# Optimization experiments

Hardware: AMD Instinct MI355X
Metric: run time of the kernel (lower is better)

The kernel has to match this reference:

```python
import jax, jax.numpy as jnp
import numpy as np

M, N, B, T = 512, 2048, 8192, 5
P, P_MAX = 0.012, 0.12


def setup_inputs() -> dict:
    key = jax.random.key(0)
    k1, k2 = jax.random.split(key)
    A = jax.random.normal(k1, (M, N), dtype=jnp.float32) / np.float32(np.sqrt(M))
    y = jax.random.normal(k2, (B, M), dtype=jnp.float32)
    # norm = 1.001 * ||A^T A||_2 (largest singular value), as in __init__
    norm = np.float32(1.001 * np.linalg.norm(np.asarray(A).T @ np.asarray(A), 2))
    beta = jnp.ones((T + 1, 1, 1), jnp.float32) * (np.float32(0.1) / norm)
    mu = jnp.ones((T + 1, 1, 1), jnp.float32) / norm
    W = A.T  # Linear weight overwritten with A.T; W(y) = y @ W.T = y @ A
    return {"y": y, "A": A, "W": W, "beta": beta, "mu": mu}


def _shrink(x, beta, t):
    # top-p hard-threshold with softshrink fallback
    abs_x = jnp.abs(x)
    idx = int(min(P * t, P_MAX) * x.shape[-1])  # static per unrolled step
    if idx > 0:
        thr = jax.lax.top_k(abs_x, idx)[0][:, idx - 1:idx]  # [B,1] p-th largest |x|
    else:
        thr = jnp.zeros((x.shape[0], 1), x.dtype)
    u = x / beta
    x_soft = beta * (jnp.sign(u) * jnp.maximum(jnp.abs(u) - 1.0, 0.0))  # beta*softshrink(x/beta,1)
    return jnp.where(abs_x >= thr, x, x_soft)


def reference(y, A, W, beta, mu):
    # W(v) = v @ W.T ; W initialized to A.T so W(y) = y @ A
    h = mu[0] * (y @ W.T)            # [B, N]
    x = _shrink(h, beta[0], 0)
    for t in range(1, T + 1):
        r = x @ A.T - y              # [B, M] residual
        k = mu[t] * (r @ W.T)        # [B, N]
        x = _shrink(x - k, beta[t], t)
    return x
```

## Files before the change

kernel.cpp:

```cpp
#include <hip/hip_runtime.h>


typedef int int4v __attribute__((ext_vector_type(4)));

__device__ __forceinline__ void quant2(float v, float inv_s,
                                       signed char& q1, signed char& q0) {
    int q = __float2int_rn(v * inv_s);
    q = q > 16256 ? 16256 : (q < -16256 ? -16256 : q);
    int hi = (q + 64) >> 7;
    q1 = (signed char)hi;
    q0 = (signed char)(q - (hi << 7));
}

__device__ __forceinline__ void gl_lds16(const signed char* g, signed char* lds) {
    __builtin_amdgcn_global_load_lds(
        (const __attribute__((address_space(1))) void*)g,
        (__attribute__((address_space(3))) void*)lds, 16, 0, 0);
}

template<int NJ, int EPI>
__global__ __launch_bounds__(256, 2) void gemm_i8(
    const signed char* __restrict__ A1, const signed char* __restrict__ A0, int lda,
    const signed char* __restrict__ B1, const signed char* __restrict__ B0, int ldb,
    const float* __restrict__ sAv,
    const float* __restrict__ sBv,
    const float* __restrict__ Yaux,
    float* __restrict__ outF,
    const float* __restrict__ muPtr, int muIdx, int K, int ldOut)
{
    constexpr int BN = 32 * NJ;
    __shared__ signed char As1[2][128 * 64];
    __shared__ signed char As0[2][128 * 64];
    __shared__ signed char Bs1[2][BN * 64];
    __shared__ signed char Bs0[2][BN * 64];

    const int tid  = threadIdx.x;
    const int wid  = tid >> 6;
    const int lane = tid & 63;
    const int quad = lane >> 4;
    const int l16  = lane & 15;
    const int waveM = (wid >> 1) * 64;
    const int waveN = (wid & 1) * (16 * NJ);
    const int swz   = (l16 >> 1) & 3;

    const int flat  = blockIdx.x + gridDim.x * blockIdx.y;
    const int mBase = (flat & 63) * 128;
    const int nBase = (flat >> 6) * BN;

    int4v accH[4][NJ] = {};
    int4v accM[4][NJ] = {};

    auto stage = [&](int b, int k0) {
        #pragma unroll
        for (int rr = 0; rr < 2; ++rr) {
            int c   = rr * 256 + tid;
            int row = c >> 2;
            int js  = (c & 3) ^ ((row >> 1) & 3);
            size_t ga = (size_t)(mBase + row) * lda + k0 + js * 16;
            size_t doff = (size_t)((rr * 256 + wid * 64) * 16);
            gl_lds16(A1 + ga, As1[b] + doff);
            gl_lds16(A0 + ga, As0[b] + doff);
        }
        #pragma unroll
        for (int rr = 0; rr < BN / 64; ++rr) {
            int c   = rr * 256 + tid;
            int row = c >> 2;
            int js  = (c & 3) ^ ((row >> 1) & 3);
            size_t gb = (size_t)(nBase + row) * ldb + k0 + js * 16;
            size_t doff = (size_t)((rr * 256 + wid * 64) * 16);
            gl_lds16(B1 + gb, Bs1[b] + doff);
            gl_lds16(B0 + gb, Bs0[b] + doff);
        }
    };

    const int KT = K >> 6;
    stage(0, 0);

    for (int kt = 0; kt < KT; ++kt) {
        const int cur = kt & 1;
        if (kt + 1 < KT) {
            stage(cur ^ 1, (kt + 1) << 6);
            if constexpr (NJ == 4) asm volatile("s_waitcnt vmcnt(8)" ::: "memory");
            else                   asm volatile("s_waitcnt vmcnt(6)" ::: "memory");
        } else {
            asm volatile("s_waitcnt vmcnt(0)" ::: "memory");
        }
        __builtin_amdgcn_s_barrier();

        int4v a1[4], a0[4], b1[NJ], b0[NJ];
        #pragma unroll
        for (int i = 0; i < 4; ++i) {
            int off = (waveM + i * 16 + l16) * 64 + ((quad ^ swz) * 16);
            a1[i] = *(const int4v*)(&As1[cur][off]);
            a0[i] = *(const int4v*)(&As0[cur][off]);
        }
        #pragma unroll
        for (int j = 0; j < NJ; ++j) {
            int off = (waveN + j * 16 + l16) * 64 + ((quad ^ swz) * 16);
            b1[j] = *(const int4v*)(&Bs1[cur][off]);
            b0[j] = *(const int4v*)(&Bs0[cur][off]);
        }
        __builtin_amdgcn_s_setprio(1);
        #pragma unroll
        for (int i = 0; i < 4; ++i)
            #pragma unroll
            for (int j = 0; j < NJ; ++j) {
                accH[i][j] = __builtin_amdgcn_mfma_i32_16x16x64_i8(a1[i], b1[j], accH[i][j], 0, 0, 0);
                accM[i][j] = __builtin_amdgcn_mfma_i32_16x16x64_i8(a1[i], b0[j], accM[i][j], 0, 0, 0);
                accM[i][j] = __builtin_amdgcn_mfma_i32_16x16x64_i8(a0[i], b1[j], accM[i][j], 0, 0, 0);
            }
        __builtin_amdgcn_s_setprio(0);
        __builtin_amdgcn_s_barrier();
    }

    const float mu = muPtr[muIdx];
    #pragma unroll
    for (int i = 0; i < 4; ++i) {
        #pragma unroll
        for (int j = 0; j < NJ; ++j) {
            const int gr0 = mBase + waveM + i * 16 + quad * 4;
            const int gc  = nBase + waveN + j * 16 + l16;
            const float sB = sBv[gc];
            #pragma unroll
            for (int r2 = 0; r2 < 4; ++r2) {
                const int    gr  = gr0 + r2;
                const size_t idx = (size_t)gr * ldOut + gc;
                const float  sA  = sAv[gr];
                float v = sA * sB * ((float)accH[i][j][r2] * 16384.f
                                   + (float)accM[i][j][r2] * 128.f);
                if constexpr (EPI == 0)      outF[idx] = mu * v;
                else if constexpr (EPI == 1) outF[idx] = v - Yaux[idx];
                else                         outF[idx] = Yaux[idx] - mu * v;
            }
        }
    }
}

template<int COLS>
__global__ __launch_bounds__(256) void rowquant_kernel(
    const float* __restrict__ src,
    signed char* __restrict__ q1, signed char* __restrict__ q0,
    float* __restrict__ scale)
{
    const int wid  = threadIdx.x >> 6;
    const int lane = threadIdx.x & 63;
    const long long row = (long long)blockIdx.x * 4 + wid;
    constexpr int EP = COLS / 256;
    const float* s = src + row * COLS;

    float v[EP * 4];
    #pragma unroll
    for (int c = 0; c < EP; ++c) {
        float4 f = ((const float4*)s)[c * 64 + lane];
        v[c * 4 + 0] = f.x; v[c * 4 + 1] = f.y; v[c * 4 + 2] = f.z; v[c * 4 + 3] = f.w;
    }
    float mx = 0.f;
    #pragma unroll
    for (int i = 0; i < EP * 4; ++i) mx = fmaxf(mx, fabsf(v[i]));
    #pragma unroll
    for (int off = 32; off >= 1; off >>= 1) mx = fmaxf(mx, __shfl_xor(mx, off, 64));
    mx = fmaxf(mx, 1e-20f);
    if (lane == 0) scale[row] = mx / 16256.f;
    const float inv = 16256.f / mx;

    #pragma unroll
    for (int c = 0; c < EP; ++c) {
        size_t col = (size_t)(c * 64 + lane) * 4;
        signed char h[4], l[4];
        #pragma unroll
        for (int e = 0; e < 4; ++e) quant2(v[c * 4 + e], inv, h[e], l[e]);
        *(char4*)(q1 + row * COLS + col) = *(char4*)h;
        *(char4*)(q0 + row * COLS + col) = *(char4*)l;
    }
}

__global__ __launch_bounds__(256) void shrink_kernel(
    float* __restrict__ z,
    signed char* __restrict__ X1, signed char* __restrict__ X0,
    float* __restrict__ sX,
    const float* __restrict__ betaPtr, int tIdx, int kSel, int writeF32)
{
    const int wid  = threadIdx.x >> 6;
    const int lane = threadIdx.x & 63;
    const long long row = (long long)blockIdx.x * 4 + wid;
    float* zr = z + row * 2048;

    float v[32];
    #pragma unroll
    for (int c = 0; c < 8; ++c) {
        float4 f = ((const float4*)zr)[c * 64 + lane];
        v[c * 4 + 0] = f.x; v[c * 4 + 1] = f.y; v[c * 4 + 2] = f.z; v[c * 4 + 3] = f.w;
    }

    if (kSel > 0) {
        const float beta = betaPtr[tIdx];
        unsigned a[32];
        #pragma unroll
        for (int i = 0; i < 32; ++i) a[i] = __float_as_uint(fabsf(v[i]));

        unsigned lo = 0u, hi = 0x7F800000u;
        for (int it = 0; it < 31; ++it) {
            unsigned mid = (lo + hi) >> 1;
            int cnt = 0;
            #pragma unroll
            for (int i = 0; i < 32; ++i) cnt += (a[i] >= mid) ? 1 : 0;
            #pragma unroll
            for (int off = 32; off >= 1; off >>= 1) cnt += __shfl_xor(cnt, off, 64);
            if (cnt >= kSel) lo = mid; else hi = mid;
        }
        const unsigned thr = lo;
        #pragma unroll
        for (int i = 0; i < 32; ++i) {
            if (a[i] < thr) {
                float av   = __uint_as_float(a[i]);
                float soft = fmaxf(av - beta, 0.f);
                v[i] = copysignf(soft, v[i]);
            }
        }
    }

    float mx = 0.f;
    #pragma unroll
    for (int i = 0; i < 32; ++i) mx = fmaxf(mx, fabsf(v[i]));
    #pragma unroll
    for (int off = 32; off >= 1; off >>= 1) mx = fmaxf(mx, __shfl_xor(mx, off, 64));
    mx = fmaxf(mx, 1e-20f);
    if (lane == 0) sX[row] = mx / 16256.f;
    const float inv = 16256.f / mx;

    #pragma unroll
    for (int c = 0; c < 8; ++c) {
        size_t col = (size_t)(c * 64 + lane) * 4;
        signed char h[4], l[4];
        #pragma unroll
        for (int e = 0; e < 4; ++e) quant2(v[c * 4 + e], inv, h[e], l[e]);
        *(char4*)(X1 + row * 2048 + col) = *(char4*)h;
        *(char4*)(X0 + row * 2048 + col) = *(char4*)l;
        if (writeF32) {
            float4 f;
            f.x = v[c * 4 + 0]; f.y = v[c * 4 + 1]; f.z = v[c * 4 + 2]; f.w = v[c * 4 + 3];
            ((float4*)zr)[c * 64 + lane] = f;
        }
    }
}

extern "C" void kernel_launch(void* const* d_in, const int* in_sizes, int n_in,
                              void* d_out, int out_size, void* d_ws, size_t ws_size,
                              hipStream_t stream)
{
    const float* y    = (const float*)d_in[0];
    const float* A    = (const float*)d_in[1];
    const float* W    = (const float*)d_in[2];
    const float* beta = (const float*)d_in[3];
    const float* mu   = (const float*)d_in[4];
    float* out = (float*)d_out;

    signed char* A1q  = (signed char*)d_ws;
    signed char* A0q  = A1q  + 512 * 2048;
    signed char* AT1q = A0q  + 512 * 2048;
    signed char* AT0q = AT1q + 2048 * 512;
    signed char* y1q  = AT0q + 2048 * 512;
    signed char* y0q  = y1q  + 8192 * 512;
    signed char* x1q  = y0q  + 8192 * 512;
    signed char* x0q  = x1q  + (size_t)8192 * 2048;
    signed char* r1q  = x0q  + (size_t)8192 * 2048;
    signed char* r0q  = r1q  + 8192 * 512;
    float* rF  = (float*)(r0q + 8192 * 512);
    float* sa  = rF + (size_t)8192 * 512;
    float* sat = sa  + 512;
    float* sy  = sat + 2048;
    float* sx  = sy  + 8192;
    float* sr  = sx  + 8192;

    rowquant_kernel<2048><<<128, 256, 0, stream>>>(A, A1q, A0q, sa);
    rowquant_kernel<512><<<512, 256, 0, stream>>>(W, AT1q, AT0q, sat);
    rowquant_kernel<512><<<2048, 256, 0, stream>>>(y, y1q, y0q, sy);

    gemm_i8<4, 0><<<dim3(16, 64), 256, 0, stream>>>(
        y1q, y0q, 512, AT1q, AT0q, 512, sy, sat,
        nullptr, out, mu, 0, 512, 2048);
    shrink_kernel<<<2048, 256, 0, stream>>>(out, x1q, x0q, sx, beta, 0, 0, 0);

    for (int t = 1; t <= 5; ++t) {
        double p = 0.012 * t; if (p > 0.12) p = 0.12;
        int kSel = (int)(p * 2048.0);

        gemm_i8<2, 1><<<dim3(8, 64), 256, 0, stream>>>(
            x1q, x0q, 2048, A1q, A0q, 2048, sx, sa,
            y, rF, mu, t, 2048, 512);
        rowquant_kernel<512><<<2048, 256, 0, stream>>>(rF, r1q, r0q, sr);

        gemm_i8<4, 2><<<dim3(16, 64), 256, 0, stream>>>(
            r1q, r0q, 512, AT1q, AT0q, 512, sr, sat,
            out, out, mu, t, 512, 2048);

        shrink_kernel<<<2048, 256, 0, stream>>>(out, x1q, x0q, sx, beta, t, kSel, 1);
    }
}
```

Baseline: 798.1 us.

## Process two rows per wave in shrink and skip final quantized plane writes

```diff
diff --git a/kernel.cpp b/kernel.cpp
--- a/kernel.cpp
+++ b/kernel.cpp
@@ -178,68 +178,124 @@
     float* __restrict__ z,
     signed char* __restrict__ X1, signed char* __restrict__ X0,
     float* __restrict__ sX,
-    const float* __restrict__ betaPtr, int tIdx, int kSel, int writeF32)
+    const float* __restrict__ betaPtr, int tIdx, int kSel,
+    int writeF32, int writePlanes)
 {
     const int wid  = threadIdx.x >> 6;
     const int lane = threadIdx.x & 63;
-    const long long row = (long long)blockIdx.x * 4 + wid;
-    float* zr = z + row * 2048;
-
-    float v[32];
+    const long long r0 = (long long)blockIdx.x * 8 + wid * 2;
+    float* z0 = z + r0 * 2048;
+    float* z1 = z0 + 2048;
+
+    unsigned a0[32], a1[32];
+    unsigned s0 = 0, s1 = 0;
     #pragma unroll
     for (int c = 0; c < 8; ++c) {
-        float4 f = ((const float4*)zr)[c * 64 + lane];
-        v[c * 4 + 0] = f.x; v[c * 4 + 1] = f.y; v[c * 4 + 2] = f.z; v[c * 4 + 3] = f.w;
+        float4 f0 = ((const float4*)z0)[c * 64 + lane];
+        float4 f1 = ((const float4*)z1)[c * 64 + lane];
+        const float e0[4] = {f0.x, f0.y, f0.z, f0.w};
+        const float e1[4] = {f1.x, f1.y, f1.z, f1.w};
+        #pragma unroll
+        for (int e = 0; e < 4; ++e) {
+            unsigned b0 = __float_as_uint(e0[e]);
+            unsigned b1 = __float_as_uint(e1[e]);
+            s0 |= (b0 >> 31) << (c * 4 + e);
+            s1 |= (b1 >> 31) << (c * 4 + e);
+            a0[c * 4 + e] = b0 & 0x7FFFFFFFu;
+            a1[c * 4 + e] = b1 & 0x7FFFFFFFu;
+        }
     }
 
     if (kSel > 0) {
         const float beta = betaPtr[tIdx];
-        unsigned a[32];
-        #pragma unroll
-        for (int i = 0; i < 32; ++i) a[i] = __float_as_uint(fabsf(v[i]));
-
-        unsigned lo = 0u, hi = 0x7F800000u;
+        unsigned lo0 = 0u, hi0 = 0x7F800000u;
+        unsigned lo1 = 0u, hi1 = 0x7F800000u;
         for (int it = 0; it < 31; ++it) {
-            unsigned mid = (lo + hi) >> 1;
-            int cnt = 0;
+            const unsigned m0 = (lo0 + hi0) >> 1;
+            const unsigned m1 = (lo1 + hi1) >> 1;
+            int c0 = 0, c1 = 0;
             #pragma unroll
-            for (int i = 0; i < 32; ++i) cnt += (a[i] >= mid) ? 1 : 0;
+            for (int i = 0; i < 32; ++i) {
+                c0 += (a0[i] >= m0) ? 1 : 0;
+                c1 += (a1[i] >= m1) ? 1 : 0;
+            }
+            int pk = c0 | (c1 << 16);
             #pragma unroll
-            for (int off = 32; off >= 1; off >>= 1) cnt += __shfl_xor(cnt, off, 64);
-            if (cnt >= kSel) lo = mid; else hi = mid;
-        }
-        const unsigned thr = lo;
+            for (int off = 32; off >= 1; off >>= 1) pk += __shfl_xor(pk, off, 64);
+            if ((pk & 0xFFFF) >= kSel) lo0 = m0; else hi0 = m0;
+            if ((pk >> 16)    >= kSel) lo1 = m1; else hi1 = m1;
+        }
+        const unsigned thr0 = lo0, thr1 = lo1;
         #pragma unroll
         for (int i = 0; i < 32; ++i) {
-            if (a[i] < thr) {
-                float av   = __uint_as_float(a[i]);
-                float soft = fmaxf(av - beta, 0.f);
-                v[i] = copysignf(soft, v[i]);
-            }
-        }
-    }
-
-    float mx = 0.f;
-    #pragma unroll
-    for (int i = 0; i < 32; ++i) mx = fmaxf(mx, fabsf(v[i]));
-    #pragma unroll
-    for (int off = 32; off >= 1; off >>= 1) mx = fmaxf(mx, __shfl_xor(mx, off, 64));
-    mx = fmaxf(mx, 1e-20f);
-    if (lane == 0) sX[row] = mx / 16256.f;
-    const float inv = 16256.f / mx;
+            float af0 = __uint_as_float(a0[i]);
+            float af1 = __uint_as_float(a1[i]);
+            unsigned sf0 = __float_as_uint(fmaxf(af0 - beta, 0.f));
+            unsigned sf1 = __float_as_uint(fmaxf(af1 - beta, 0.f));
+            a0[i] = (a0[i] >= thr0) ? a0[i] : sf0;
+            a1[i] = (a1[i] >= thr1) ? a1[i] : sf1;
+        }
+    }
+
+    unsigned mx0 = 0u, mx1 = 0u;
+    #pragma unroll
+    for (int i = 0; i < 32; ++i) {
+        mx0 = a0[i] > mx0 ? a0[i] : mx0;
+        mx1 = a1[i] > mx1 ? a1[i] : mx1;
+    }
+    #pragma unroll
+    for (int off = 32; off >= 1; off >>= 1) {
+        unsigned t0 = (unsigned)__shfl_xor((int)mx0, off, 64);
+        unsigned t1 = (unsigned)__shfl_xor((int)mx1, off, 64);
+        mx0 = t0 > mx0 ? t0 : mx0;
+        mx1 = t1 > mx1 ? t1 : mx1;
+    }
+    const float fm0 = fmaxf(__uint_as_float(mx0), 1e-20f);
+    const float fm1 = fmaxf(__uint_as_float(mx1), 1e-20f);
+    if (writePlanes && lane == 0) {
+        sX[r0]     = fm0 / 16256.f;
+        sX[r0 + 1] = fm1 / 16256.f;
+    }
+    const float inv0 = 16256.f / fm0;
+    const float inv1 = 16256.f / fm1;
 
     #pragma unroll
     for (int c = 0; c < 8; ++c) {
-        size_t col = (size_t)(c * 64 + lane) * 4;
-        signed char h[4], l[4];
-        #pragma unroll
-        for (int e = 0; e < 4; ++e) quant2(v[c * 4 + e], inv, h[e], l[e]);
-        *(char4*)(X1 + row * 2048 + col) = *(char4*)h;
-        *(char4*)(X0 + row * 2048 + col) = *(char4*)l;
+        const size_t col = (size_t)(c * 64 + lane) * 4;
+        signed char h0[4], l0[4], h1[4], l1[4];
+        float w0[4], w1[4];
+        #pragma unroll
+        for (int e = 0; e < 4; ++e) {
+            const int i = c * 4 + e;
+            const unsigned sg0 = (s0 >> i) & 1u;
+            const unsigned sg1 = (s1 >> i) & 1u;
+            const float av0 = __uint_as_float(a0[i]);
+            const float av1 = __uint_as_float(a1[i]);
+            w0[e] = __uint_as_float(a0[i] | (sg0 << 31));
+            w1[e] = __uint_as_float(a1[i] | (sg1 << 31));
+            int q0i = __float2int_rn(av0 * inv0);
+            int q1i = __float2int_rn(av1 * inv1);
+            q0i = q0i > 16256 ? 16256 : q0i;
+            q1i = q1i > 16256 ? 16256 : q1i;
+            q0i = sg0 ? -q0i : q0i;
+            q1i = sg1 ? -q1i : q1i;
+            int hi0b = (q0i + 64) >> 7;
+            int hi1b = (q1i + 64) >> 7;
+            h0[e] = (signed char)hi0b;  l0[e] = (signed char)(q0i - (hi0b << 7));
+            h1[e] = (signed char)hi1b;  l1[e] = (signed char)(q1i - (hi1b << 7));
+        }
+        if (writePlanes) {
+            *(char4*)(X1 + r0 * 2048 + col)       = *(char4*)h0;
+            *(char4*)(X0 + r0 * 2048 + col)       = *(char4*)l0;
+            *(char4*)(X1 + (r0 + 1) * 2048 + col) = *(char4*)h1;
+            *(char4*)(X0 + (r0 + 1) * 2048 + col) = *(char4*)l1;
+        }
         if (writeF32) {
-            float4 f;
-            f.x = v[c * 4 + 0]; f.y = v[c * 4 + 1]; f.z = v[c * 4 + 2]; f.w = v[c * 4 + 3];
-            ((float4*)zr)[c * 64 + lane] = f;
+            float4 f0, f1;
+            f0.x = w0[0]; f0.y = w0[1]; f0.z = w0[2]; f0.w = w0[3];
+            f1.x = w1[0]; f1.y = w1[1]; f1.z = w1[2]; f1.w = w1[3];
+            ((float4*)z0)[c * 64 + lane] = f0;
+            ((float4*)z1)[c * 64 + lane] = f1;
         }
     }
 }
@@ -279,7 +335,7 @@
     gemm_i8<4, 0><<<dim3(16, 64), 256, 0, stream>>>(
         y1q, y0q, 512, AT1q, AT0q, 512, sy, sat,
         nullptr, out, mu, 0, 512, 2048);
-    shrink_kernel<<<2048, 256, 0, stream>>>(out, x1q, x0q, sx, beta, 0, 0, 0);
+    shrink_kernel<<<1024, 256, 0, stream>>>(out, x1q, x0q, sx, beta, 0, 0, 0, 1);
 
     for (int t = 1; t <= 5; ++t) {
         double p = 0.012 * t; if (p > 0.12) p = 0.12;
@@ -294,6 +350,7 @@
             r1q, r0q, 512, AT1q, AT0q, 512, sr, sat,
             out, out, mu, t, 512, 2048);
 
-        shrink_kernel<<<2048, 256, 0, stream>>>(out, x1q, x0q, sx, beta, t, kSel, 1);
-    }
-}
+        shrink_kernel<<<1024, 256, 0, stream>>>(out, x1q, x0q, sx, beta, t,
+                                                kSel, 1, t < 5 ? 1 : 0);
+    }
+}
```

Result: slower. 870.8 us (+9.1%).
